# Performance work log

Hardware: AMD Instinct MI355X
Metric: run time of the kernel (lower is better)

## Reference

```python
import jax, jax.numpy as jnp
import numpy as np

d_model = 512


def setup_inputs() -> dict:
    key = jax.random.key(0)
    k1, k2, k3, k4 = jax.random.split(key, 4)
    B, T, d_k = 8, 2048, 64
    scale = 1.0 / np.sqrt(d_model)
    x = jax.random.normal(k1, (B, T, d_model), dtype=jnp.float32)
    Wk = jax.random.normal(k2, (d_model, d_k), dtype=jnp.float32) * scale
    Wq = jax.random.normal(k3, (d_model, d_k), dtype=jnp.float32) * scale
    Wv = jax.random.normal(k4, (d_model, d_k), dtype=jnp.float32) * scale
    return {"x": x, "Wk": Wk, "Wq": Wq, "Wv": Wv}


def reference(x, Wk, Wq, Wv):
    # x: [B,T,C]; W*: [C,d_k]  (torch Linear weight is [d_k,C]; we store transposed)
    k = jnp.einsum('btc,cd->btd', x, Wk)
    q = jnp.einsum('btc,cd->btd', x, Wq)
    v = jnp.einsum('btc,cd->btd', x, Wv)
    d_k = k.shape[-1]
    scores = jnp.einsum('bqd,bkd->bqk', q, k) / jnp.sqrt(jnp.float32(d_k))
    attn = jax.nn.softmax(scores, axis=-1)  # [B,T,T]
    return jnp.einsum('bqk,bkd->bqd', attn, v)
```

## Files before the change

kernel.cpp:

```cpp
#include <hip/hip_runtime.h>
#include <hip/hip_bf16.h>
#include <stdint.h>


typedef short bf16x8 __attribute__((ext_vector_type(8)));
typedef float f32x4 __attribute__((ext_vector_type(4)));

#define MFMA_BF16 __builtin_amdgcn_mfma_f32_16x16x32_bf16

__device__ __forceinline__ unsigned int pk2(float a, float b) {
    __hip_bfloat162 h = __float22bfloat162_rn(float2{a, b});
    union { __hip_bfloat162 h; unsigned int u; } r; r.h = h;
    return r.u;
}

__device__ __forceinline__ uint2 pack4_bf16(float a, float b, float c, float d) {
    uint2 r; r.x = pk2(a, b); r.y = pk2(c, d); return r;
}

__device__ __forceinline__ bf16x8 cvt8(f32x4 a, f32x4 b) {
    union { bf16x8 v; unsigned int u[4]; } r;
    r.u[0] = pk2(a[0], a[1]); r.u[1] = pk2(a[2], a[3]);
    r.u[2] = pk2(b[0], b[1]); r.u[3] = pk2(b[2], b[3]);
    return r.v;
}

__device__ __forceinline__ unsigned short bf1(float a) {
    __hip_bfloat16 h = __float2bfloat16(a);
    union { __hip_bfloat16 h; unsigned short u; } r; r.h = h;
    return r.u;
}

__global__ void wt_kernel(const float* __restrict__ Wq,
                          const float* __restrict__ Wk,
                          const float* __restrict__ Wv,
                          unsigned short* __restrict__ wt2)
{
    int id = blockIdx.x * 256 + threadIdx.x;
    int c    = id & 15;
    int quad = (id >> 4) & 3;
    int ks   = (id >> 6) & 15;
    int mt   = (id >> 10) & 3;
    int w    = id >> 12;
    const float* src = (w == 0) ? Wq : ((w == 1) ? Wk : Wv);
    const int n  = mt * 16 + c;
    const int k0 = ks * 32 + quad * 8;
    unsigned short* dst = wt2 + (size_t)id * 8;
    #pragma unroll
    for (int j = 0; j < 8; j++)
        dst[j] = bf1(src[(size_t)(k0 + j) * 64 + n]);
}

__global__ void xconv_kernel(const float* __restrict__ x,
                             unsigned short* __restrict__ xb2)
{
    int i = blockIdx.x * 256 + threadIdx.x;
    int tok    = i >> 6;
    int dblock = i & 63;
    f32x4 a = *(const f32x4*)(x + (size_t)i * 8);
    f32x4 b = *(const f32x4*)(x + (size_t)i * 8 + 4);
    int tt = tok >> 4, c = tok & 15;
    int ks = dblock >> 2, quad = dblock & 3;
    size_t chunk = ((size_t)(tt * 16 + ks) * 4 + quad) * 16 + c;
    *(bf16x8*)(xb2 + chunk * 8) = cvt8(a, b);
}

__global__ __launch_bounds__(256, 1) void proj_kernel(
    const unsigned short* __restrict__ xb2, const unsigned short* __restrict__ wt2,
    unsigned short* __restrict__ qg, unsigned short* __restrict__ kg2,
    unsigned short* __restrict__ vg2)
{
    const int lane = threadIdx.x & 63;
    const int c    = lane & 15;
    const int quad = lane >> 4;
    const int wave = threadIdx.x >> 6;
    const int gw   = blockIdx.x * 4 + wave;
    const int w    = gw % 3;
    const int tt   = gw / 3;
    const int t0   = tt * 16;

    f32x4 acc[4];
    #pragma unroll
    for (int i = 0; i < 4; i++) acc[i] = f32x4{0.f, 0.f, 0.f, 0.f};

    const unsigned short* xbase = xb2 + ((size_t)tt * 16 * 64 + lane) * 8;
    const unsigned short* wbase = wt2 + ((size_t)w * 4 * 16 * 64 + lane) * 8;

    #pragma unroll 4
    for (int ks = 0; ks < 16; ks++) {
        bf16x8 xf = *(const bf16x8*)(xbase + (size_t)ks * 64 * 8);
        #pragma unroll
        for (int mt = 0; mt < 4; mt++) {
            bf16x8 wa = *(const bf16x8*)(wbase + ((size_t)mt * 16 + ks) * 64 * 8);
            acc[mt] = MFMA_BF16(wa, xf, acc[mt], 0, 0, 0);
        }
    }

    const int b  = t0 >> 11;
    const int tb = t0 & 2047;

    if (w == 0) {
        unsigned short* base = qg + (size_t)(t0 + c) * 64;
        #pragma unroll
        for (int mt = 0; mt < 4; mt++)
            *(uint2*)(base + mt * 16 + quad * 4) =
                pack4_bf16(acc[mt][0], acc[mt][1], acc[mt][2], acc[mt][3]);
    } else if (w == 1) {
        const int g = tb >> 4;
        #pragma unroll
        for (int mt = 0; mt < 4; mt++) {
            const int h  = mt >> 1;
            const int qk = (mt & 1) * 2 + (quad >> 1);
            size_t chunk = (size_t)b * 16384 + ((size_t)(g * 2 + h) * 4 + qk) * 16 + c;
            *(uint2*)(kg2 + chunk * 8 + (quad & 1) * 4) =
                pack4_bf16(acc[mt][0], acc[mt][1], acc[mt][2], acc[mt][3]);
        }
    } else {
        const int tk = tb + c;
        const int s  = tk >> 5;
        const int qv = (tk >> 3) & 3;
        const int j  = tk & 7;
        #pragma unroll
        for (int mt = 0; mt < 4; mt++) {
            size_t chunk = (size_t)b * 16384 + ((size_t)(s * 4 + mt) * 4 + qv) * 16 + quad * 4;
            unsigned short* dst = vg2 + chunk * 8 + j;
            dst[0]  = bf1(acc[mt][0]);
            dst[8]  = bf1(acc[mt][1]);
            dst[16] = bf1(acc[mt][2]);
            dst[24] = bf1(acc[mt][3]);
        }
    }
}

__global__ __launch_bounds__(256, 1) void attn_kernel(
    const unsigned short* __restrict__ qg, const unsigned short* __restrict__ kg2,
    const unsigned short* __restrict__ vg2, float* __restrict__ out)
{
    __shared__ unsigned short pt[4][16 * 136];
    __shared__ float obuf[4][16][68];
    __shared__ float lbuf[4][16];

    const int lane = threadIdx.x & 63;
    const int wave = threadIdx.x >> 6;
    const int c    = lane & 15;
    const int quad = lane >> 4;
    const int b    = blockIdx.x & 7;
    const int ti   = blockIdx.x >> 3;
    const int t0   = b * 2048 + ti * 16;

    unsigned short* ptw = &pt[wave][0];
    const unsigned short* kbase = kg2 + ((size_t)b * 16384 + lane) * 8;
    const unsigned short* vbase = vg2 + ((size_t)b * 16384 + lane) * 8;

    bf16x8 qb0 = *(const bf16x8*)(qg + (size_t)(t0 + c) * 64 + quad * 8);
    bf16x8 qb1 = *(const bf16x8*)(qg + (size_t)(t0 + c) * 64 + 32 + quad * 8);

    f32x4 o0 = {0,0,0,0}, o1 = {0,0,0,0}, o2 = {0,0,0,0}, o3 = {0,0,0,0};
    f32x4 lacc = {0,0,0,0};
    const float cexp = 0.18033688011112042f;

    for (int kt = wave * 4; kt < wave * 4 + 4; kt++) {
        const int key0 = kt * 128;
        const int g0   = key0 >> 4;
        const int s0   = key0 >> 5;

        f32x4 st[8];
        const f32x4 z = {0,0,0,0};
        #pragma unroll
        for (int mt = 0; mt < 8; mt++) {
            bf16x8 k0 = *(const bf16x8*)(kbase + (size_t)((g0 + mt) * 2    ) * 64 * 8);
            bf16x8 k1 = *(const bf16x8*)(kbase + (size_t)((g0 + mt) * 2 + 1) * 64 * 8);
            st[mt] = MFMA_BF16(k0, qb0, z, 0, 0, 0);
            st[mt] = MFMA_BF16(k1, qb1, st[mt], 0, 0, 0);
        }

        bf16x8 va[2][4];
        #pragma unroll
        for (int mt = 0; mt < 4; mt++) {
            va[0][mt] = *(const bf16x8*)(vbase + (size_t)((s0    ) * 4 + mt) * 64 * 8);
            va[1][mt] = *(const bf16x8*)(vbase + (size_t)((s0 + 1) * 4 + mt) * 64 * 8);
        }

        asm volatile("" ::: "memory");
        #pragma unroll
        for (int mt = 0; mt < 8; mt++) {
            float p0 = __builtin_amdgcn_exp2f(st[mt][0] * cexp);
            float p1 = __builtin_amdgcn_exp2f(st[mt][1] * cexp);
            float p2 = __builtin_amdgcn_exp2f(st[mt][2] * cexp);
            float p3 = __builtin_amdgcn_exp2f(st[mt][3] * cexp);
            lacc[0] += p0; lacc[1] += p1; lacc[2] += p2; lacc[3] += p3;
            *(uint2*)(ptw + c * 136 + mt * 16 + quad * 4) = pack4_bf16(p0, p1, p2, p3);
        }
        asm volatile("" ::: "memory");

        #pragma unroll
        for (int ks = 0; ks < 4; ks++) {
            bf16x8 pb = *(const bf16x8*)(ptw + c * 136 + ks * 32 + quad * 8);
            bf16x8 v0 = va[ks & 1][0], v1 = va[ks & 1][1];
            bf16x8 v2 = va[ks & 1][2], v3 = va[ks & 1][3];
            if (ks < 2) {
                #pragma unroll
                for (int mt = 0; mt < 4; mt++)
                    va[ks & 1][mt] =
                        *(const bf16x8*)(vbase + (size_t)((s0 + ks + 2) * 4 + mt) * 64 * 8);
            }
            o0 = MFMA_BF16(v0, pb, o0, 0, 0, 0);
            o1 = MFMA_BF16(v1, pb, o1, 0, 0, 0);
            o2 = MFMA_BF16(v2, pb, o2, 0, 0, 0);
            o3 = MFMA_BF16(v3, pb, o3, 0, 0, 0);
        }
        asm volatile("" ::: "memory");
    }

    float l = (lacc[0] + lacc[1]) + (lacc[2] + lacc[3]);
    l += __shfl_xor(l, 16);
    l += __shfl_xor(l, 32);

    *(f32x4*)&obuf[wave][c][ 0 + quad * 4] = o0;
    *(f32x4*)&obuf[wave][c][16 + quad * 4] = o1;
    *(f32x4*)&obuf[wave][c][32 + quad * 4] = o2;
    *(f32x4*)&obuf[wave][c][48 + quad * 4] = o3;
    if (quad == 0) lbuf[wave][c] = l;
    __syncthreads();

    const int tid = threadIdx.x;
    const int q   = tid >> 4;
    const int d0  = (tid & 15) * 4;
    const float L = (lbuf[0][q] + lbuf[1][q]) + (lbuf[2][q] + lbuf[3][q]);
    f32x4 O = {0.f, 0.f, 0.f, 0.f};
    #pragma unroll
    for (int w = 0; w < 4; w++) {
        f32x4 ov = *(const f32x4*)&obuf[w][q][d0];
        O[0] += ov[0]; O[1] += ov[1]; O[2] += ov[2]; O[3] += ov[3];
    }
    const float rl = 1.f / L;
    O[0] *= rl; O[1] *= rl; O[2] *= rl; O[3] *= rl;
    *(f32x4*)(out + (size_t)(t0 + q) * 64 + d0) = O;
}

extern "C" void kernel_launch(void* const* d_in, const int* in_sizes, int n_in,
                              void* d_out, int out_size, void* d_ws, size_t ws_size,
                              hipStream_t stream)
{
    const float* x  = (const float*)d_in[0];
    const float* Wk = (const float*)d_in[1];
    const float* Wq = (const float*)d_in[2];
    const float* Wv = (const float*)d_in[3];
    float* out = (float*)d_out;

    char* ws = (char*)d_ws;
    unsigned short* qg  = (unsigned short*)(ws);
    unsigned short* kg2 = (unsigned short*)(ws + (2u << 20));
    unsigned short* vg2 = (unsigned short*)(ws + (4u << 20));
    unsigned short* wt2 = (unsigned short*)(ws + (6u << 20));
    unsigned short* xb2 = (unsigned short*)(ws + (7u << 20));

    hipLaunchKernelGGL(wt_kernel,    dim3(48),   dim3(256), 0, stream, Wq, Wk, Wv, wt2);
    hipLaunchKernelGGL(xconv_kernel, dim3(4096), dim3(256), 0, stream, x, xb2);
    hipLaunchKernelGGL(proj_kernel,  dim3(768),  dim3(256), 0, stream, xb2, wt2, qg, kg2, vg2);
    hipLaunchKernelGGL(attn_kernel,  dim3(1024), dim3(256), 0, stream, qg, kg2, vg2, out);
}
```

Before: 115.3 us.

## Split attention blocks into two query tiles and two key halves per block

Each attention block now handles 32 query rows, with two waves per 16-row query tile, each covering half of the keys (8 key tiles instead of 4). The grid halves to 512 blocks, and the cross-wave reduction combines only two partials per row. The projection kernel is also remapped so each block uses a single weight matrix across four token tiles, which improves weight reuse in cache. The trade-off is fewer blocks (512 on a GPU with many CUs) and a longer serial loop per wave, which may cut occupancy and latency hiding.

```diff
diff --git a/kernel.cpp b/kernel.cpp
--- a/kernel.cpp
+++ b/kernel.cpp
@@ -74,9 +74,8 @@
     const int c    = lane & 15;
     const int quad = lane >> 4;
     const int wave = threadIdx.x >> 6;
-    const int gw   = blockIdx.x * 4 + wave;
-    const int w    = gw % 3;
-    const int tt   = gw / 3;
+    const int w    = blockIdx.x % 3;
+    const int tt   = (blockIdx.x / 3) * 4 + wave;
     const int t0   = tt * 16;
 
     f32x4 acc[4];
@@ -145,8 +144,11 @@
     const int c    = lane & 15;
     const int quad = lane >> 4;
     const int b    = blockIdx.x & 7;
-    const int ti   = blockIdx.x >> 3;
-    const int t0   = b * 2048 + ti * 16;
+    const int g    = blockIdx.x >> 3;
+    const int qi   = wave & 1;
+    const int h    = wave >> 1;
+    const int tb   = b * 2048 + g * 32;
+    const int t0   = tb + qi * 16;
 
     unsigned short* ptw = &pt[wave][0];
     const unsigned short* kbase = kg2 + ((size_t)b * 16384 + lane) * 8;
@@ -159,7 +161,7 @@
     f32x4 lacc = {0,0,0,0};
     const float cexp = 0.18033688011112042f;
 
-    for (int kt = wave * 4; kt < wave * 4 + 4; kt++) {
+    for (int kt = h * 8; kt < h * 8 + 8; kt++) {
         const int key0 = kt * 128;
         const int g0   = key0 >> 4;
         const int s0   = key0 >> 5;
@@ -224,18 +226,26 @@
     __syncthreads();
 
     const int tid = threadIdx.x;
-    const int q   = tid >> 4;
-    const int d0  = (tid & 15) * 4;
-    const float L = (lbuf[0][q] + lbuf[1][q]) + (lbuf[2][q] + lbuf[3][q]);
-    f32x4 O = {0.f, 0.f, 0.f, 0.f};
-    #pragma unroll
-    for (int w = 0; w < 4; w++) {
-        f32x4 ov = *(const f32x4*)&obuf[w][q][d0];
-        O[0] += ov[0]; O[1] += ov[1]; O[2] += ov[2]; O[3] += ov[3];
-    }
+    const int qr  = tid >> 3;
+    const int d0  = (tid & 7) * 8;
+    const int q2  = qr >> 4;
+    const int q16 = qr & 15;
+    const float L = lbuf[q2][q16] + lbuf[q2 + 2][q16];
     const float rl = 1.f / L;
-    O[0] *= rl; O[1] *= rl; O[2] *= rl; O[3] *= rl;
-    *(f32x4*)(out + (size_t)(t0 + q) * 64 + d0) = O;
+    f32x4 Oa, Ob;
+    {
+        f32x4 a0 = *(const f32x4*)&obuf[q2][q16][d0];
+        f32x4 a1 = *(const f32x4*)&obuf[q2 + 2][q16][d0];
+        f32x4 b0 = *(const f32x4*)&obuf[q2][q16][d0 + 4];
+        f32x4 b1 = *(const f32x4*)&obuf[q2 + 2][q16][d0 + 4];
+        Oa[0]=(a0[0]+a1[0])*rl; Oa[1]=(a0[1]+a1[1])*rl;
+        Oa[2]=(a0[2]+a1[2])*rl; Oa[3]=(a0[3]+a1[3])*rl;
+        Ob[0]=(b0[0]+b1[0])*rl; Ob[1]=(b0[1]+b1[1])*rl;
+        Ob[2]=(b0[2]+b1[2])*rl; Ob[3]=(b0[3]+b1[3])*rl;
+    }
+    float* op = out + (size_t)(tb + qr) * 64 + d0;
+    *(f32x4*)op       = Oa;
+    *(f32x4*)(op + 4) = Ob;
 }
 
 extern "C" void kernel_launch(void* const* d_in, const int* in_sizes, int n_in,
@@ -258,5 +268,5 @@
     hipLaunchKernelGGL(wt_kernel,    dim3(48),   dim3(256), 0, stream, Wq, Wk, Wv, wt2);
     hipLaunchKernelGGL(xconv_kernel, dim3(4096), dim3(256), 0, stream, x, xb2);
     hipLaunchKernelGGL(proj_kernel,  dim3(768),  dim3(256), 0, stream, xb2, wt2, qg, kg2, vg2);
-    hipLaunchKernelGGL(attn_kernel,  dim3(1024), dim3(256), 0, stream, qg, kg2, vg2, out);
-}
+    hipLaunchKernelGGL(attn_kernel,  dim3(512),  dim3(256), 0, stream, qg, kg2, vg2, out);
+}
```

Result: slower. 122.7 us (+6.4%).

## Process two query tiles per attention block and merge weight/x conversion kernels

Applied to the files above, without the earlier changes.

Each attention block now handles 32 query rows, two 16-row tiles, so every loaded K and V fragment feeds twice as many MFMAs. This halves global K/V traffic per query and halves the grid from 1024 to 512 blocks. Separately, the weight-transpose and x-conversion kernels are merged into one launch to save a kernel launch. The trade-off is more registers and LDS per block and fewer blocks to spread across CUs.

```diff
diff --git a/kernel.cpp b/kernel.cpp
--- a/kernel.cpp
+++ b/kernel.cpp
@@ -31,30 +31,30 @@
     return r.u;
 }
 
-__global__ void wt_kernel(const float* __restrict__ Wq,
-                          const float* __restrict__ Wk,
-                          const float* __restrict__ Wv,
-                          unsigned short* __restrict__ wt2)
-{
-    int id = blockIdx.x * 256 + threadIdx.x;
-    int c    = id & 15;
-    int quad = (id >> 4) & 3;
-    int ks   = (id >> 6) & 15;
-    int mt   = (id >> 10) & 3;
-    int w    = id >> 12;
-    const float* src = (w == 0) ? Wq : ((w == 1) ? Wk : Wv);
-    const int n  = mt * 16 + c;
-    const int k0 = ks * 32 + quad * 8;
-    unsigned short* dst = wt2 + (size_t)id * 8;
-    #pragma unroll
-    for (int j = 0; j < 8; j++)
-        dst[j] = bf1(src[(size_t)(k0 + j) * 64 + n]);
-}
-
-__global__ void xconv_kernel(const float* __restrict__ x,
-                             unsigned short* __restrict__ xb2)
-{
-    int i = blockIdx.x * 256 + threadIdx.x;
+__global__ void prep_kernel(const float* __restrict__ x,
+                            const float* __restrict__ Wq,
+                            const float* __restrict__ Wk,
+                            const float* __restrict__ Wv,
+                            unsigned short* __restrict__ xb2,
+                            unsigned short* __restrict__ wt2)
+{
+    if (blockIdx.x < 48) {
+        int id = blockIdx.x * 256 + threadIdx.x;
+        int c    = id & 15;
+        int quad = (id >> 4) & 3;
+        int ks   = (id >> 6) & 15;
+        int mt   = (id >> 10) & 3;
+        int w    = id >> 12;
+        const float* src = (w == 0) ? Wq : ((w == 1) ? Wk : Wv);
+        const int n  = mt * 16 + c;
+        const int k0 = ks * 32 + quad * 8;
+        unsigned short* dst = wt2 + (size_t)id * 8;
+        #pragma unroll
+        for (int j = 0; j < 8; j++)
+            dst[j] = bf1(src[(size_t)(k0 + j) * 64 + n]);
+        return;
+    }
+    int i = (blockIdx.x - 48) * 256 + threadIdx.x;
     int tok    = i >> 6;
     int dblock = i & 63;
     f32x4 a = *(const f32x4*)(x + (size_t)i * 8);
@@ -136,27 +136,30 @@
     const unsigned short* __restrict__ qg, const unsigned short* __restrict__ kg2,
     const unsigned short* __restrict__ vg2, float* __restrict__ out)
 {
-    __shared__ unsigned short pt[4][16 * 136];
-    __shared__ float obuf[4][16][68];
-    __shared__ float lbuf[4][16];
+    __shared__ unsigned short pt[4][2][16 * 136];
+    __shared__ float obuf[4][2][16][68];
+    __shared__ float lbuf[4][2][16];
 
     const int lane = threadIdx.x & 63;
     const int wave = threadIdx.x >> 6;
     const int c    = lane & 15;
     const int quad = lane >> 4;
     const int b    = blockIdx.x & 7;
-    const int ti   = blockIdx.x >> 3;
-    const int t0   = b * 2048 + ti * 16;
-
-    unsigned short* ptw = &pt[wave][0];
+    const int g    = blockIdx.x >> 3;
+    const int tb   = b * 2048 + g * 32;
+
+    unsigned short* ptw = &pt[wave][0][0];
     const unsigned short* kbase = kg2 + ((size_t)b * 16384 + lane) * 8;
     const unsigned short* vbase = vg2 + ((size_t)b * 16384 + lane) * 8;
 
-    bf16x8 qb0 = *(const bf16x8*)(qg + (size_t)(t0 + c) * 64 + quad * 8);
-    bf16x8 qb1 = *(const bf16x8*)(qg + (size_t)(t0 + c) * 64 + 32 + quad * 8);
-
-    f32x4 o0 = {0,0,0,0}, o1 = {0,0,0,0}, o2 = {0,0,0,0}, o3 = {0,0,0,0};
-    f32x4 lacc = {0,0,0,0};
+    bf16x8 qa0 = *(const bf16x8*)(qg + (size_t)(tb + c) * 64 + quad * 8);
+    bf16x8 qa1 = *(const bf16x8*)(qg + (size_t)(tb + c) * 64 + 32 + quad * 8);
+    bf16x8 qc0 = *(const bf16x8*)(qg + (size_t)(tb + 16 + c) * 64 + quad * 8);
+    bf16x8 qc1 = *(const bf16x8*)(qg + (size_t)(tb + 16 + c) * 64 + 32 + quad * 8);
+
+    f32x4 oa0 = {0,0,0,0}, oa1 = {0,0,0,0}, oa2 = {0,0,0,0}, oa3 = {0,0,0,0};
+    f32x4 ob0 = {0,0,0,0}, ob1 = {0,0,0,0}, ob2 = {0,0,0,0}, ob3 = {0,0,0,0};
+    f32x4 laccA = {0,0,0,0}, laccB = {0,0,0,0};
     const float cexp = 0.18033688011112042f;
 
     for (int kt = wave * 4; kt < wave * 4 + 4; kt++) {
@@ -164,14 +167,16 @@
         const int g0   = key0 >> 4;
         const int s0   = key0 >> 5;
 
-        f32x4 st[8];
+        f32x4 stA[8], stB[8];
         const f32x4 z = {0,0,0,0};
         #pragma unroll
         for (int mt = 0; mt < 8; mt++) {
             bf16x8 k0 = *(const bf16x8*)(kbase + (size_t)((g0 + mt) * 2    ) * 64 * 8);
             bf16x8 k1 = *(const bf16x8*)(kbase + (size_t)((g0 + mt) * 2 + 1) * 64 * 8);
-            st[mt] = MFMA_BF16(k0, qb0, z, 0, 0, 0);
-            st[mt] = MFMA_BF16(k1, qb1, st[mt], 0, 0, 0);
+            stA[mt] = MFMA_BF16(k0, qa0, z, 0, 0, 0);
+            stA[mt] = MFMA_BF16(k1, qa1, stA[mt], 0, 0, 0);
+            stB[mt] = MFMA_BF16(k0, qc0, z, 0, 0, 0);
+            stB[mt] = MFMA_BF16(k1, qc1, stB[mt], 0, 0, 0);
         }
 
         bf16x8 va[2][4];
@@ -184,18 +189,28 @@
         asm volatile("" ::: "memory");
         #pragma unroll
         for (int mt = 0; mt < 8; mt++) {
-            float p0 = __builtin_amdgcn_exp2f(st[mt][0] * cexp);
-            float p1 = __builtin_amdgcn_exp2f(st[mt][1] * cexp);
-            float p2 = __builtin_amdgcn_exp2f(st[mt][2] * cexp);
-            float p3 = __builtin_amdgcn_exp2f(st[mt][3] * cexp);
-            lacc[0] += p0; lacc[1] += p1; lacc[2] += p2; lacc[3] += p3;
+            float p0 = __builtin_amdgcn_exp2f(stA[mt][0] * cexp);
+            float p1 = __builtin_amdgcn_exp2f(stA[mt][1] * cexp);
+            float p2 = __builtin_amdgcn_exp2f(stA[mt][2] * cexp);
+            float p3 = __builtin_amdgcn_exp2f(stA[mt][3] * cexp);
+            laccA[0] += p0; laccA[1] += p1; laccA[2] += p2; laccA[3] += p3;
             *(uint2*)(ptw + c * 136 + mt * 16 + quad * 4) = pack4_bf16(p0, p1, p2, p3);
         }
+        #pragma unroll
+        for (int mt = 0; mt < 8; mt++) {
+            float p0 = __builtin_amdgcn_exp2f(stB[mt][0] * cexp);
+            float p1 = __builtin_amdgcn_exp2f(stB[mt][1] * cexp);
+            float p2 = __builtin_amdgcn_exp2f(stB[mt][2] * cexp);
+            float p3 = __builtin_amdgcn_exp2f(stB[mt][3] * cexp);
+            laccB[0] += p0; laccB[1] += p1; laccB[2] += p2; laccB[3] += p3;
+            *(uint2*)(ptw + 2176 + c * 136 + mt * 16 + quad * 4) = pack4_bf16(p0, p1, p2, p3);
+        }
         asm volatile("" ::: "memory");
 
         #pragma unroll
         for (int ks = 0; ks < 4; ks++) {
-            bf16x8 pb = *(const bf16x8*)(ptw + c * 136 + ks * 32 + quad * 8);
+            bf16x8 pbA = *(const bf16x8*)(ptw + c * 136 + ks * 32 + quad * 8);
+            bf16x8 pbB = *(const bf16x8*)(ptw + 2176 + c * 136 + ks * 32 + quad * 8);
             bf16x8 v0 = va[ks & 1][0], v1 = va[ks & 1][1];
             bf16x8 v2 = va[ks & 1][2], v3 = va[ks & 1][3];
             if (ks < 2) {
@@ -204,38 +219,57 @@
                     va[ks & 1][mt] =
                         *(const bf16x8*)(vbase + (size_t)((s0 + ks + 2) * 4 + mt) * 64 * 8);
             }
-            o0 = MFMA_BF16(v0, pb, o0, 0, 0, 0);
-            o1 = MFMA_BF16(v1, pb, o1, 0, 0, 0);
-            o2 = MFMA_BF16(v2, pb, o2, 0, 0, 0);
-            o3 = MFMA_BF16(v3, pb, o3, 0, 0, 0);
+            oa0 = MFMA_BF16(v0, pbA, oa0, 0, 0, 0);
+            oa1 = MFMA_BF16(v1, pbA, oa1, 0, 0, 0);
+            oa2 = MFMA_BF16(v2, pbA, oa2, 0, 0, 0);
+            oa3 = MFMA_BF16(v3, pbA, oa3, 0, 0, 0);
+            ob0 = MFMA_BF16(v0, pbB, ob0, 0, 0, 0);
+            ob1 = MFMA_BF16(v1, pbB, ob1, 0, 0, 0);
+            ob2 = MFMA_BF16(v2, pbB, ob2, 0, 0, 0);
+            ob3 = MFMA_BF16(v3, pbB, ob3, 0, 0, 0);
         }
         asm volatile("" ::: "memory");
     }
 
-    float l = (lacc[0] + lacc[1]) + (lacc[2] + lacc[3]);
-    l += __shfl_xor(l, 16);
-    l += __shfl_xor(l, 32);
-
-    *(f32x4*)&obuf[wave][c][ 0 + quad * 4] = o0;
-    *(f32x4*)&obuf[wave][c][16 + quad * 4] = o1;
-    *(f32x4*)&obuf[wave][c][32 + quad * 4] = o2;
-    *(f32x4*)&obuf[wave][c][48 + quad * 4] = o3;
-    if (quad == 0) lbuf[wave][c] = l;
+    float lA = (laccA[0] + laccA[1]) + (laccA[2] + laccA[3]);
+    lA += __shfl_xor(lA, 16);
+    lA += __shfl_xor(lA, 32);
+    float lB = (laccB[0] + laccB[1]) + (laccB[2] + laccB[3]);
+    lB += __shfl_xor(lB, 16);
+    lB += __shfl_xor(lB, 32);
+
+    *(f32x4*)&obuf[wave][0][c][ 0 + quad * 4] = oa0;
+    *(f32x4*)&obuf[wave][0][c][16 + quad * 4] = oa1;
+    *(f32x4*)&obuf[wave][0][c][32 + quad * 4] = oa2;
+    *(f32x4*)&obuf[wave][0][c][48 + quad * 4] = oa3;
+    *(f32x4*)&obuf[wave][1][c][ 0 + quad * 4] = ob0;
+    *(f32x4*)&obuf[wave][1][c][16 + quad * 4] = ob1;
+    *(f32x4*)&obuf[wave][1][c][32 + quad * 4] = ob2;
+    *(f32x4*)&obuf[wave][1][c][48 + quad * 4] = ob3;
+    if (quad == 0) { lbuf[wave][0][c] = lA; lbuf[wave][1][c] = lB; }
     __syncthreads();
 
     const int tid = threadIdx.x;
-    const int q   = tid >> 4;
-    const int d0  = (tid & 15) * 4;
-    const float L = (lbuf[0][q] + lbuf[1][q]) + (lbuf[2][q] + lbuf[3][q]);
-    f32x4 O = {0.f, 0.f, 0.f, 0.f};
+    const int row = tid >> 3;
+    const int d0  = (tid & 7) * 8;
+    const int qt  = row >> 4;
+    const int r   = row & 15;
+    const float L = (lbuf[0][qt][r] + lbuf[1][qt][r]) +
+                    (lbuf[2][qt][r] + lbuf[3][qt][r]);
+    const float rl = 1.f / L;
+    f32x4 Oa = {0,0,0,0}, Ob = {0,0,0,0};
     #pragma unroll
     for (int w = 0; w < 4; w++) {
-        f32x4 ov = *(const f32x4*)&obuf[w][q][d0];
-        O[0] += ov[0]; O[1] += ov[1]; O[2] += ov[2]; O[3] += ov[3];
-    }
-    const float rl = 1.f / L;
-    O[0] *= rl; O[1] *= rl; O[2] *= rl; O[3] *= rl;
-    *(f32x4*)(out + (size_t)(t0 + q) * 64 + d0) = O;
+        f32x4 a = *(const f32x4*)&obuf[w][qt][r][d0];
+        f32x4 bfr = *(const f32x4*)&obuf[w][qt][r][d0 + 4];
+        Oa[0] += a[0]; Oa[1] += a[1]; Oa[2] += a[2]; Oa[3] += a[3];
+        Ob[0] += bfr[0]; Ob[1] += bfr[1]; Ob[2] += bfr[2]; Ob[3] += bfr[3];
+    }
+    Oa[0] *= rl; Oa[1] *= rl; Oa[2] *= rl; Oa[3] *= rl;
+    Ob[0] *= rl; Ob[1] *= rl; Ob[2] *= rl; Ob[3] *= rl;
+    float* op = out + (size_t)(tb + row) * 64 + d0;
+    *(f32x4*)op       = Oa;
+    *(f32x4*)(op + 4) = Ob;
 }
 
 extern "C" void kernel_launch(void* const* d_in, const int* in_sizes, int n_in,
@@ -255,8 +289,10 @@
     unsigned short* wt2 = (unsigned short*)(ws + (6u << 20));
     unsigned short* xb2 = (unsigned short*)(ws + (7u << 20));
 
-    hipLaunchKernelGGL(wt_kernel,    dim3(48),   dim3(256), 0, stream, Wq, Wk, Wv, wt2);
-    hipLaunchKernelGGL(xconv_kernel, dim3(4096), dim3(256), 0, stream, x, xb2);
-    hipLaunchKernelGGL(proj_kernel,  dim3(768),  dim3(256), 0, stream, xb2, wt2, qg, kg2, vg2);
-    hipLaunchKernelGGL(attn_kernel,  dim3(1024), dim3(256), 0, stream, qg, kg2, vg2, out);
-}
+    hipLaunchKernelGGL(prep_kernel, dim3(4144), dim3(256), 0, stream,
+                       x, Wq, Wk, Wv, xb2, wt2);
+    hipLaunchKernelGGL(proj_kernel, dim3(768),  dim3(256), 0, stream,
+                       xb2, wt2, qg, kg2, vg2);
+    hipLaunchKernelGGL(attn_kernel, dim3(512),  dim3(256), 0, stream,
+                       qg, kg2, vg2, out);
+}
```

New measurement: 110.2 us. -4.4%, faster.
